# Kernel tuning notes

Measured on AMD Instinct MI355X. Metric: run time of the kernel, lower is better.

The kernel has to match this reference:

```python
import math
import jax, jax.numpy as jnp
import numpy as np

N_HEADS, INPUT_DIM, EMBED_DIM = 8, 512, 512
KEY_DIM = EMBED_DIM // N_HEADS  # 64, val_dim == key_dim
BATCH, N = 4, 2048


def setup_inputs() -> dict:
    key = jax.random.key(0)
    ks = jax.random.split(key, 6)
    def unif(k, shape):
        stdv = 1.0 / math.sqrt(shape[-1])
        return jax.random.uniform(k, shape, jnp.float32, -stdv, stdv)
    q = jax.random.normal(ks[0], (BATCH, N, INPUT_DIM), jnp.float32)
    mask = jax.random.randint(ks[1], (BATCH, N, N), 0, 2, jnp.int32)
    W_query = unif(ks[2], (N_HEADS, INPUT_DIM, KEY_DIM))
    W_key = unif(ks[3], (N_HEADS, INPUT_DIM, KEY_DIM))
    W_val = unif(ks[4], (N_HEADS, INPUT_DIM, KEY_DIM))
    W_out = unif(ks[5], (N_HEADS, KEY_DIM, EMBED_DIM))
    return {"q": q, "mask": mask, "W_query": W_query, "W_key": W_key,
            "W_val": W_val, "W_out": W_out}


def reference(q, mask, W_query, W_key, W_val, W_out):
    # Self-attention: k is None, v is None -> k = q, v = q (module forward_).
    norm = 1.0 / math.sqrt(KEY_DIM)
    m = mask.astype(bool)[None]  # (1, b, nq, ng) broadcast over heads
    Q = jnp.einsum('bnd,hdk->hbnk', q, W_query)  # (h, b, nq, dk)
    K = jnp.einsum('bnd,hdk->hbnk', q, W_key)    # (h, b, ng, dk)
    V = jnp.einsum('bnd,hdv->hbnv', q, W_val)    # (h, b, ng, dv)
    scores = norm * jnp.einsum('hbqk,hbgk->hbqg', Q, K)  # (h, b, nq, ng)
    scores = jnp.where(m, -jnp.inf, scores)
    attn = jax.nn.softmax(scores, axis=-1)
    attn = jnp.where(m, 0.0, attn)  # zero out masked (also kills NaN rows)
    heads = jnp.einsum('hbqg,hbgv->hbqv', attn, V)
    out = jnp.einsum('hbqv,hve->bqe', heads, W_out)  # (b, nq, embed)
    return out
```

## Files before the change

### kernel.cpp

```cpp
#include <hip/hip_runtime.h>
#include <hip/hip_bf16.h>
#include <stdint.h>

using bf16 = __hip_bfloat16;
typedef __attribute__((ext_vector_type(8))) short short8;
typedef __attribute__((ext_vector_type(4))) short short4b;
typedef __attribute__((ext_vector_type(4))) float f32x4;
typedef __attribute__((ext_vector_type(4))) unsigned int u32x4;

#if __has_builtin(__builtin_amdgcn_exp2f)
#define EXP2(x) __builtin_amdgcn_exp2f(x)
#else
#define EXP2(x) exp2f(x)
#endif

__device__ __forceinline__ short8 load8(const bf16* p) {
  return *reinterpret_cast<const short8*>(p);
}
__device__ __forceinline__ short f2b(float f) {
  return __builtin_bit_cast(short, __float2bfloat16(f));
}
__device__ __forceinline__ unsigned int pk2(float a, float b) {
  return (unsigned int)(unsigned short)f2b(a) |
         ((unsigned int)(unsigned short)f2b(b) << 16);
}
__device__ __forceinline__ void asy16(const bf16* g, bf16* l) {
  __builtin_amdgcn_global_load_lds(
      (const __attribute__((address_space(1))) void*)g,
      (__attribute__((address_space(3))) void*)l, 16, 0, 0);
}


__global__ void k_prep(const float4* __restrict__ x, ushort4* __restrict__ xb,
                       const float* __restrict__ Wq, const float* __restrict__ Wk,
                       const float* __restrict__ Wv, const float* __restrict__ Wo,
                       bf16* __restrict__ Wcat, bf16* __restrict__ Wot,
                       const int4* __restrict__ m4,
                       unsigned long long* __restrict__ bits) {
  int blk = blockIdx.x;
  const int tid = threadIdx.x;
  if (blk < 4096) {
    int i = blk * 256 + tid;
    float4 v = x[i];
    ushort4 o;
    o.x = (unsigned short)f2b(v.x);
    o.y = (unsigned short)f2b(v.y);
    o.z = (unsigned short)f2b(v.z);
    o.w = (unsigned short)f2b(v.w);
    xb[i] = o;
  } else if (blk < 4352) {
    int t = blk - 4096;
    __shared__ float T[64][65];
    if (t < 192) {
      int which = t >> 6;
      int h = (t >> 3) & 7, dt = t & 7;
      const float* W = (which == 0) ? Wq : ((which == 1) ? Wk : Wv);
#pragma unroll
      for (int p = 0; p < 4; ++p) {
        int row = p * 16 + (tid >> 4);
        float4 v = *(const float4*)(W + (size_t)(h * 512 + dt * 64 + row) * 64 +
                                    (tid & 15) * 4);
        T[row][(tid & 15) * 4 + 0] = v.x;
        T[row][(tid & 15) * 4 + 1] = v.y;
        T[row][(tid & 15) * 4 + 2] = v.z;
        T[row][(tid & 15) * 4 + 3] = v.w;
      }
      __syncthreads();
      float scale = (which == 0) ? 0.18033688011112042f : 1.0f;
      int jj = tid >> 2, i0 = (tid & 3) * 16;
#pragma unroll
      for (int q = 0; q < 2; ++q) {
        short8 o;
#pragma unroll
        for (int e = 0; e < 8; ++e) o[e] = f2b(T[i0 + q * 8 + e][jj] * scale);
        *(short8*)(Wcat + (size_t)(which * 512 + h * 64 + jj) * 512 + dt * 64 +
                   i0 + q * 8) = o;
      }
    } else {
      int t2 = t - 192;
      int h = t2 >> 3, et = t2 & 7;
#pragma unroll
      for (int p = 0; p < 4; ++p) {
        int row = p * 16 + (tid >> 4);
        float4 v = *(const float4*)(Wo + (size_t)(h * 64 + row) * 512 + et * 64 +
                                    (tid & 15) * 4);
        T[row][(tid & 15) * 4 + 0] = v.x;
        T[row][(tid & 15) * 4 + 1] = v.y;
        T[row][(tid & 15) * 4 + 2] = v.z;
        T[row][(tid & 15) * 4 + 3] = v.w;
      }
      __syncthreads();
      int jj = tid >> 2, i0 = (tid & 3) * 16;
#pragma unroll
      for (int q = 0; q < 2; ++q) {
        short8 o;
#pragma unroll
        for (int e = 0; e < 8; ++e) o[e] = f2b(T[i0 + q * 8 + e][jj]);
        *(short8*)(Wot + (size_t)(et * 64 + jj) * 512 + h * 64 + i0 + q * 8) = o;
      }
    }
  } else {
    int i = (blk - 4352) * 256 + tid;
    int4 v = m4[i];
    unsigned int nib = (unsigned)(v.x != 0) | ((unsigned)(v.y != 0) << 1) |
                       ((unsigned)(v.z != 0) << 2) | ((unsigned)(v.w != 0) << 3);
    unsigned long long w = (unsigned long long)nib << (4 * (tid & 15));
    w |= __shfl_xor(w, 1);
    w |= __shfl_xor(w, 2);
    w |= __shfl_xor(w, 4);
    w |= __shfl_xor(w, 8);
    if ((tid & 15) == 0) bits[i >> 4] = w;
  }
}

__device__ __forceinline__ void gemm128(const bf16* __restrict__ A,
                                        const bf16* __restrict__ Bt,
                                        bf16* As, bf16* Bs,
                                        int rowBase, int colBase,
                                        f32x4 acc[4][4]) {
  const int tid = threadIdx.x;
  const int lane = tid & 63, w = tid >> 6;
  const int g = lane >> 4, r = lane & 15;

  auto stage = [&](int buf, int s) {
#pragma unroll
    for (int p = 0; p < 2; ++p) {
      int c = p * 256 + tid;
      int row = c >> 2, gr = c & 3, sg = gr ^ (row & 3);
      asy16(A + (size_t)(rowBase + row) * 512 + s * 32 + sg * 8,
            As + buf * 4096 + c * 8);
    }
#pragma unroll
    for (int p = 0; p < 2; ++p) {
      int c = p * 256 + tid;
      int row = c >> 2, gr = c & 3, sg = gr ^ (row & 3);
      asy16(Bt + (size_t)(colBase + row) * 512 + s * 32 + sg * 8,
            Bs + buf * 4096 + c * 8);
    }
  };

  stage(0, 0);
  int buf = 0;
  const int rbl = (w >> 1) * 64, cbl = (w & 1) * 64;
  for (int s = 0; s < 16; ++s) {
    __syncthreads();
    if (s < 15) stage(buf ^ 1, s + 1);
    const bf16* a0 = As + buf * 4096;
    const bf16* b0 = Bs + buf * 4096;
    short8 af[4], bfr[4];
#pragma unroll
    for (int mt = 0; mt < 4; ++mt) {
      int row = rbl + mt * 16 + r;
      af[mt] = load8(a0 + (row * 4 + (g ^ (row & 3))) * 8);
    }
#pragma unroll
    for (int nt = 0; nt < 4; ++nt) {
      int col = cbl + nt * 16 + r;
      bfr[nt] = load8(b0 + (col * 4 + (g ^ (col & 3))) * 8);
    }
#pragma unroll
    for (int mt = 0; mt < 4; ++mt)
#pragma unroll
      for (int nt = 0; nt < 4; ++nt)
        acc[mt][nt] = __builtin_amdgcn_mfma_f32_16x16x32_bf16(
            af[mt], bfr[nt], acc[mt][nt], 0, 0, 0);
    buf ^= 1;
  }
}

__device__ __forceinline__ void gemm64x128(const bf16* __restrict__ A,
                                           const bf16* __restrict__ Bt,
                                           bf16* As, bf16* Bs,
                                           int rowBase, int colBase,
                                           f32x4 acc[2][4]) {
  const int tid = threadIdx.x;
  const int lane = tid & 63, w = tid >> 6;
  const int g = lane >> 4, r = lane & 15;

  auto stage = [&](int buf, int s) {
    {
      int c = tid;
      int row = c >> 2, gr = c & 3, sg = gr ^ (row & 3);
      asy16(A + (size_t)(rowBase + row) * 512 + s * 32 + sg * 8,
            As + buf * 2048 + c * 8);
    }
#pragma unroll
    for (int p = 0; p < 2; ++p) {
      int c = p * 256 + tid;
      int row = c >> 2, gr = c & 3, sg = gr ^ (row & 3);
      asy16(Bt + (size_t)(colBase + row) * 512 + s * 32 + sg * 8,
            Bs + buf * 4096 + c * 8);
    }
  };

  stage(0, 0);
  int buf = 0;
  const int rbl = (w >> 1) * 32, cbl = (w & 1) * 64;
  for (int s = 0; s < 16; ++s) {
    __syncthreads();
    if (s < 15) stage(buf ^ 1, s + 1);
    const bf16* a0 = As + buf * 2048;
    const bf16* b0 = Bs + buf * 4096;
    short8 af[2], bfr[4];
#pragma unroll
    for (int mt = 0; mt < 2; ++mt) {
      int row = rbl + mt * 16 + r;
      af[mt] = load8(a0 + (row * 4 + (g ^ (row & 3))) * 8);
    }
#pragma unroll
    for (int nt = 0; nt < 4; ++nt) {
      int col = cbl + nt * 16 + r;
      bfr[nt] = load8(b0 + (col * 4 + (g ^ (col & 3))) * 8);
    }
#pragma unroll
    for (int mt = 0; mt < 2; ++mt)
#pragma unroll
      for (int nt = 0; nt < 4; ++nt)
        acc[mt][nt] = __builtin_amdgcn_mfma_f32_16x16x32_bf16(
            af[mt], bfr[nt], acc[mt][nt], 0, 0, 0);
    buf ^= 1;
  }
}

__global__ __launch_bounds__(256, 3) void k_proj_qkv(
    const bf16* __restrict__ Xb, const bf16* __restrict__ Wcat,
    bf16* __restrict__ Qb, bf16* __restrict__ Kp, bf16* __restrict__ Vp) {
  __shared__ __align__(16) bf16 As[2 * 4096];
  __shared__ __align__(16) bf16 Bs[2 * 4096];
  int rowBase = blockIdx.x * 128, colBase = blockIdx.y * 128;
  f32x4 acc[4][4] = {};
  gemm128(Xb, Wcat, As, Bs, rowBase, colBase, acc);
  const int lane = threadIdx.x & 63, w = threadIdx.x >> 6;
  const int g = lane >> 4, r = lane & 15;
#pragma unroll
  for (int mt = 0; mt < 4; ++mt) {
    int row0 = rowBase + (w >> 1) * 64 + mt * 16 + 4 * g;
    int b = row0 >> 11, n0 = row0 & 2047;
    int kt = n0 >> 6;
#pragma unroll
    for (int nt = 0; nt < 4; ++nt) {
      int col = colBase + (w & 1) * 64 + nt * 16 + r;
      if (col < 512) {
        int hh = col >> 6, dk = col & 63;
        bf16* p0 = Qb + ((size_t)(b * 8 + hh) * 2048 + n0) * 64 + dk;
#pragma unroll
        for (int rr = 0; rr < 4; ++rr)
          p0[rr * 64] = __float2bfloat16(acc[mt][nt][rr]);
      } else if (col < 1024) {
        int hh = (col >> 6) & 7, dk = col & 63;
        int half = dk >> 5, gk = (dk >> 3) & 3, jj = dk & 7;
        int kr = n0 & 63;
        int kc = kr >> 4, r0 = kr & 15;
        bf16* base = Kp + (size_t)(b * 8 + hh) * 131072 + (size_t)kt * 4096 +
                     ((kc * 2 + half) * 4 + gk) * 128 + jj;
#pragma unroll
        for (int rr = 0; rr < 4; ++rr)
          base[(r0 + rr) * 8] = __float2bfloat16(acc[mt][nt][rr]);
      } else {
        int hdv = col - 1024;
        int hh = hdv >> 6, dv = hdv & 63;
        int dvs = dv >> 4, rv = dv & 15;
        int kcol0 = n0 & 63;
        int half = kcol0 >> 5, gv = (kcol0 >> 2) & 3;
        int j0 = ((kcol0 >> 4) & 1) * 4;
        short4b pkv;
#pragma unroll
        for (int rr = 0; rr < 4; ++rr) pkv[rr] = f2b(acc[mt][nt][rr]);
        *reinterpret_cast<short4b*>(
            Vp + (size_t)(b * 8 + hh) * 131072 + (size_t)kt * 4096 +
            (((half * 4 + dvs) * 4 + gv) * 16 + rv) * 8 + j0) = pkv;
      }
    }
  }
}

__global__ __launch_bounds__(256, 4) void k_proj_out(
    const bf16* __restrict__ O, const bf16* __restrict__ Wot,
    float* __restrict__ out) {
  __shared__ __align__(16) bf16 As[2 * 2048];
  __shared__ __align__(16) bf16 Bs[2 * 4096];
  int rowBase = blockIdx.x * 64, colBase = blockIdx.y * 128;
  f32x4 acc[2][4] = {};
  gemm64x128(O, Wot, As, Bs, rowBase, colBase, acc);
  const int lane = threadIdx.x & 63, w = threadIdx.x >> 6;
  const int g = lane >> 4, r = lane & 15;
#pragma unroll
  for (int mt = 0; mt < 2; ++mt) {
    int row0 = rowBase + (w >> 1) * 32 + mt * 16 + 4 * g;
#pragma unroll
    for (int nt = 0; nt < 4; ++nt) {
      int col = colBase + (w & 1) * 64 + nt * 16 + r;
#pragma unroll
      for (int rr = 0; rr < 4; ++rr)
        out[(size_t)(row0 + rr) * 512 + col] = acc[mt][nt][rr];
    }
  }
}

__global__ __launch_bounds__(512, 4) void k_attn(const bf16* __restrict__ Q,
    const bf16* __restrict__ K, const bf16* __restrict__ V,
    const unsigned long long* __restrict__ MB, bf16* __restrict__ O) {
  const int blin = blockIdx.x;
  const int j = blin >> 3;
  const int bh = (blin & 7) * 4 + (j >> 4);
  const int qt = j & 15;
  const int b = bh >> 3, h = bh & 7;
  const int tid = threadIdx.x;
  const int lane = tid & 63;
  const int wave = tid >> 6;
  const int g = lane >> 4, r = lane & 15;
  const int qbase = qt * 128 + wave * 16;

  __shared__ __align__(16) bf16 Kl[3][4096];
  __shared__ __align__(16) bf16 Vl[3][4096];

  const bf16* Kp = K + (size_t)bh * 131072;
  const bf16* Vp = V + (size_t)bh * 131072;

  short8 qf0, qf1;
  {
    const bf16* Qp = Q + ((size_t)bh * 2048 + qbase + r) * 64;
    qf0 = load8(Qp + g * 8);
    qf1 = load8(Qp + 32 + g * 8);
  }
  const unsigned long long* Mp = MB + ((size_t)b * 2048 + qbase + r) * 32;

  short8 ones;
#pragma unroll
  for (int i = 0; i < 8; ++i) ones[i] = (short)0x3F80;

  f32x4 acc[4] = {};
  f32x4 acc_l = {};

  auto stage = [&](int buf, int kt) {
    const bf16* Kg = Kp + (size_t)kt * 4096;
    const bf16* Vg = Vp + (size_t)kt * 4096;
    asy16(Kg + tid * 8, &Kl[buf][0] + tid * 8);
    asy16(Vg + tid * 8, &Vl[buf][0] + tid * 8);
  };

  auto qk = [&](const bf16* kl, f32x4 stl[4]) {
#pragma unroll
    for (int kc = 0; kc < 4; ++kc) {
      short8 kf0 = load8(kl + ((kc * 2 + 0) * 4 + g) * 128 + r * 8);
      short8 kf1 = load8(kl + ((kc * 2 + 1) * 4 + g) * 128 + r * 8);
      f32x4 z = {};
      z = __builtin_amdgcn_mfma_f32_16x16x32_bf16(kf0, qf0, z, 0, 0, 0);
      stl[kc] = __builtin_amdgcn_mfma_f32_16x16x32_bf16(kf1, qf1, z, 0, 0, 0);
    }
  };

  stage(0, 0);
  stage(1, 1);
  unsigned long long mw0, mw1;
  mw0 = Mp[0];
  __syncthreads();
  f32x4 st0[4], st1[4];
  qk(&Kl[0][0], st0);

#define ATTN_ITER(KT, CUR, NXT, STG, SC, SN, MC, MN, DO_STAGE, DO_NEXT)      \
  do {                                                                       \
    __syncthreads();                                                         \
    if (DO_STAGE) stage(STG, (KT) + 2);                                      \
    if (DO_NEXT) MN = Mp[(KT) + 1];                                          \
    __builtin_amdgcn_s_setprio(1);                                           \
    if (DO_NEXT) qk(&Kl[NXT][0], SN);                                        \
    __builtin_amdgcn_s_setprio(0);                                           \
    unsigned ml = (unsigned)MC >> (4 * g);                                   \
    unsigned mh = (unsigned)(MC >> 32) >> (4 * g);                           \
    float p[16];                                                             \
    _Pragma("unroll") for (int kc = 0; kc < 4; ++kc)                         \
        _Pragma("unroll") for (int rr = 0; rr < 4; ++rr) {                   \
      float e = EXP2(SC[kc][rr]);                                            \
      unsigned wsel = (kc & 2) ? mh : ml;                                    \
      bool bad = (wsel >> (((kc & 1) << 4) + rr)) & 1u;                      \
      p[kc * 4 + rr] = bad ? 0.f : e;                                        \
    }                                                                        \
    u32x4 q0, q1;                                                            \
    _Pragma("unroll") for (int i2 = 0; i2 < 4; ++i2) {                       \
      q0[i2] = pk2(p[2 * i2], p[2 * i2 + 1]);                                \
      q1[i2] = pk2(p[8 + 2 * i2], p[8 + 2 * i2 + 1]);                        \
    }                                                                        \
    short8 pa0 = __builtin_bit_cast(short8, q0);                             \
    short8 pa1 = __builtin_bit_cast(short8, q1);                             \
    acc_l = __builtin_amdgcn_mfma_f32_16x16x32_bf16(pa0, ones, acc_l, 0, 0, 0); \
    acc_l = __builtin_amdgcn_mfma_f32_16x16x32_bf16(pa1, ones, acc_l, 0, 0, 0); \
    const bf16* vl = &Vl[CUR][0];                                            \
    __builtin_amdgcn_s_setprio(1);                                           \
    _Pragma("unroll") for (int dvs = 0; dvs < 4; ++dvs) {                    \
      short8 vb0 = load8(vl + ((0 * 4 + dvs) * 4 + g) * 128 + r * 8);        \
      short8 vb1 = load8(vl + ((1 * 4 + dvs) * 4 + g) * 128 + r * 8);        \
      acc[dvs] = __builtin_amdgcn_mfma_f32_16x16x32_bf16(pa0, vb0, acc[dvs], 0, 0, 0); \
      acc[dvs] = __builtin_amdgcn_mfma_f32_16x16x32_bf16(pa1, vb1, acc[dvs], 0, 0, 0); \
    }                                                                        \
    __builtin_amdgcn_s_setprio(0);                                           \
  } while (0)

  for (int t = 0; t < 5; ++t) {
    const int kt = 6 * t;
    ATTN_ITER(kt + 0, 0, 1, 2, st0, st1, mw0, mw1, true, true);
    ATTN_ITER(kt + 1, 1, 2, 0, st1, st0, mw1, mw0, true, true);
    ATTN_ITER(kt + 2, 2, 0, 1, st0, st1, mw0, mw1, true, true);
    ATTN_ITER(kt + 3, 0, 1, 2, st1, st0, mw1, mw0, true, true);
    ATTN_ITER(kt + 4, 1, 2, 0, st0, st1, mw0, mw1, true, true);
    ATTN_ITER(kt + 5, 2, 0, 1, st1, st0, mw1, mw0, true, true);
  }
  ATTN_ITER(30, 0, 1, 2, st0, st1, mw0, mw1, false, true);
  ATTN_ITER(31, 1, 2, 0, st1, st0, mw1, mw0, false, false);
#undef ATTN_ITER

  float inv[4];
#pragma unroll
  for (int rr = 0; rr < 4; ++rr)
    inv[rr] = (acc_l[rr] > 0.f) ? 1.f / acc_l[rr] : 0.f;
  bf16* Op = O + ((size_t)b * 2048 + qbase + 4 * g) * 512 + h * 64;
#pragma unroll
  for (int dvs = 0; dvs < 4; ++dvs)
#pragma unroll
    for (int rr = 0; rr < 4; ++rr)
      Op[rr * 512 + dvs * 16 + r] = __float2bfloat16(acc[dvs][rr] * inv[rr]);
}


extern "C" void kernel_launch(void* const* d_in, const int* in_sizes, int n_in,
                              void* d_out, int out_size, void* d_ws, size_t ws_size,
                              hipStream_t stream) {
  const float* q    = (const float*)d_in[0];
  const int*   mask = (const int*)d_in[1];
  const float* Wq   = (const float*)d_in[2];
  const float* Wk   = (const float*)d_in[3];
  const float* Wv   = (const float*)d_in[4];
  const float* Wo   = (const float*)d_in[5];
  float* out = (float*)d_out;

  char* ws = (char*)d_ws;
  const size_t MB1 = 1024 * 1024;
  bf16* Xb   = (bf16*)(ws + 0);
  bf16* Ob   = (bf16*)(ws + 0);
  bf16* Qb   = (bf16*)(ws + 8 * MB1);
  bf16* Kpm  = (bf16*)(ws + 16 * MB1);
  bf16* Vpm  = (bf16*)(ws + 24 * MB1);
  unsigned long long* Mbits = (unsigned long long*)(ws + 32 * MB1);
  bf16* Wcat = (bf16*)(ws + 34 * MB1);
  bf16* Wot  = (bf16*)(ws + 34 * MB1 + 1536 * 512 * 2);

  k_prep<<<20736, 256, 0, stream>>>((const float4*)q, (ushort4*)Xb,
                                    Wq, Wk, Wv, Wo, Wcat, Wot,
                                    (const int4*)mask, Mbits);
  k_proj_qkv<<<dim3(64, 12), 256, 0, stream>>>(Xb, Wcat, Qb, Kpm, Vpm);
  k_attn<<<512, 512, 0, stream>>>(Qb, Kpm, Vpm, Mbits, Ob);
  k_proj_out<<<dim3(128, 4), 256, 0, stream>>>(Ob, Wot, out);
}
```

Measured before the change: 205.2 us.

## Remap GEMM blocks per XCD, invert mask bits, use packed bf16 convert

The QKV and output projection GEMMs now use a 1D grid whose block index is remapped so that each XCD handles a contiguous group of row panels, which should improve L2 reuse of the A operand. The mask bitmap is stored inverted so the attention loop can zero masked probabilities with a sign-extended bitfield AND instead of a select. Float-to-bf16 packing is done with a single v_cvt_pk_bf16_f32 instruction. The s_setprio hints around the MFMA sections are removed. Together these aim to cut VALU work in the softmax inner loop and improve cache locality, at the risk of losing the scheduling benefit that the priority hints gave.

```diff
diff --git a/kernel.cpp b/kernel.cpp
--- a/kernel.cpp
+++ b/kernel.cpp
@@ -20,9 +20,18 @@
 __device__ __forceinline__ short f2b(float f) {
   return __builtin_bit_cast(short, __float2bfloat16(f));
 }
-__device__ __forceinline__ unsigned int pk2(float a, float b) {
-  return (unsigned int)(unsigned short)f2b(a) |
-         ((unsigned int)(unsigned short)f2b(b) << 16);
+__device__ __forceinline__ unsigned int cvtpk(float lo, float hi) {
+  unsigned int r;
+  asm("v_cvt_pk_bf16_f32 %0, %1, %2" : "=v"(r) : "v"(lo), "v"(hi));
+  return r;
+}
+__device__ __forceinline__ float keepmul(float e, unsigned w, int pos) {
+#if __has_builtin(__builtin_amdgcn_sbfe)
+  unsigned km = (unsigned)__builtin_amdgcn_sbfe((int)w, pos, 1);
+  return __builtin_bit_cast(float, __builtin_bit_cast(unsigned, e) & km);
+#else
+  return ((w >> pos) & 1u) ? e : 0.f;
+#endif
 }
 __device__ __forceinline__ void asy16(const bf16* g, bf16* l) {
   __builtin_amdgcn_global_load_lds(
@@ -109,7 +118,7 @@
     w |= __shfl_xor(w, 2);
     w |= __shfl_xor(w, 4);
     w |= __shfl_xor(w, 8);
-    if ((tid & 15) == 0) bits[i >> 4] = w;
+    if ((tid & 15) == 0) bits[i >> 4] = ~w;
   }
 }
 
@@ -225,9 +234,13 @@
 __global__ __launch_bounds__(256, 3) void k_proj_qkv(
     const bf16* __restrict__ Xb, const bf16* __restrict__ Wcat,
     bf16* __restrict__ Qb, bf16* __restrict__ Kp, bf16* __restrict__ Vp) {
+  const int bid = blockIdx.x;
+  const int xcd = bid & 7, idx = bid >> 3;
+  const int rowPanel = (xcd << 3) | (idx & 7);
+  const int colPanel = idx >> 3;
+  int rowBase = rowPanel * 128, colBase = colPanel * 128;
   __shared__ __align__(16) bf16 As[2 * 4096];
   __shared__ __align__(16) bf16 Bs[2 * 4096];
-  int rowBase = blockIdx.x * 128, colBase = blockIdx.y * 128;
   f32x4 acc[4][4] = {};
   gemm128(Xb, Wcat, As, Bs, rowBase, colBase, acc);
   const int lane = threadIdx.x & 63, w = threadIdx.x >> 6;
@@ -277,9 +290,13 @@
 __global__ __launch_bounds__(256, 4) void k_proj_out(
     const bf16* __restrict__ O, const bf16* __restrict__ Wot,
     float* __restrict__ out) {
+  const int bid = blockIdx.x;
+  const int xcd = bid & 7, idx = bid >> 3;
+  const int rowPanel = (xcd << 4) | (idx & 15);
+  const int colPanel = idx >> 4;
+  int rowBase = rowPanel * 64, colBase = colPanel * 128;
   __shared__ __align__(16) bf16 As[2 * 2048];
   __shared__ __align__(16) bf16 Bs[2 * 4096];
-  int rowBase = blockIdx.x * 64, colBase = blockIdx.y * 128;
   f32x4 acc[2][4] = {};
   gemm64x128(O, Wot, As, Bs, rowBase, colBase, acc);
   const int lane = threadIdx.x & 63, w = threadIdx.x >> 6;
@@ -358,42 +375,35 @@
   f32x4 st0[4], st1[4];
   qk(&Kl[0][0], st0);
 
-#define ATTN_ITER(KT, CUR, NXT, STG, SC, SN, MC, MN, DO_STAGE, DO_NEXT)      \
-  do {                                                                       \
-    __syncthreads();                                                         \
-    if (DO_STAGE) stage(STG, (KT) + 2);                                      \
-    if (DO_NEXT) MN = Mp[(KT) + 1];                                          \
-    __builtin_amdgcn_s_setprio(1);                                           \
-    if (DO_NEXT) qk(&Kl[NXT][0], SN);                                        \
-    __builtin_amdgcn_s_setprio(0);                                           \
-    unsigned ml = (unsigned)MC >> (4 * g);                                   \
-    unsigned mh = (unsigned)(MC >> 32) >> (4 * g);                           \
-    float p[16];                                                             \
-    _Pragma("unroll") for (int kc = 0; kc < 4; ++kc)                         \
-        _Pragma("unroll") for (int rr = 0; rr < 4; ++rr) {                   \
-      float e = EXP2(SC[kc][rr]);                                            \
-      unsigned wsel = (kc & 2) ? mh : ml;                                    \
-      bool bad = (wsel >> (((kc & 1) << 4) + rr)) & 1u;                      \
-      p[kc * 4 + rr] = bad ? 0.f : e;                                        \
-    }                                                                        \
-    u32x4 q0, q1;                                                            \
-    _Pragma("unroll") for (int i2 = 0; i2 < 4; ++i2) {                       \
-      q0[i2] = pk2(p[2 * i2], p[2 * i2 + 1]);                                \
-      q1[i2] = pk2(p[8 + 2 * i2], p[8 + 2 * i2 + 1]);                        \
-    }                                                                        \
-    short8 pa0 = __builtin_bit_cast(short8, q0);                             \
-    short8 pa1 = __builtin_bit_cast(short8, q1);                             \
+#define ATTN_ITER(KT, CUR, NXT, STG, SC, SN, MC, MN, DO_STAGE, DO_NEXT)       \
+  do {                                                                        \
+    __syncthreads();                                                          \
+    if (DO_STAGE) stage(STG, (KT) + 2);                                       \
+    if (DO_NEXT) MN = Mp[(KT) + 1];                                           \
+    if (DO_NEXT) qk(&Kl[NXT][0], SN);                                         \
+    unsigned ml = (unsigned)MC >> (4 * g);                                    \
+    unsigned mh = (unsigned)(MC >> 32) >> (4 * g);                            \
+    float p[16];                                                              \
+    _Pragma("unroll") for (int kc = 0; kc < 4; ++kc)                          \
+        _Pragma("unroll") for (int rr = 0; rr < 4; ++rr)                      \
+      p[kc * 4 + rr] = keepmul(EXP2(SC[kc][rr]), (kc & 2) ? mh : ml,          \
+                               ((kc & 1) << 4) + rr);                         \
+    u32x4 q0, q1;                                                             \
+    _Pragma("unroll") for (int i2 = 0; i2 < 4; ++i2) {                        \
+      q0[i2] = cvtpk(p[2 * i2], p[2 * i2 + 1]);                               \
+      q1[i2] = cvtpk(p[8 + 2 * i2], p[8 + 2 * i2 + 1]);                       \
+    }                                                                         \
+    short8 pa0 = __builtin_bit_cast(short8, q0);                              \
+    short8 pa1 = __builtin_bit_cast(short8, q1);                              \
     acc_l = __builtin_amdgcn_mfma_f32_16x16x32_bf16(pa0, ones, acc_l, 0, 0, 0); \
     acc_l = __builtin_amdgcn_mfma_f32_16x16x32_bf16(pa1, ones, acc_l, 0, 0, 0); \
-    const bf16* vl = &Vl[CUR][0];                                            \
-    __builtin_amdgcn_s_setprio(1);                                           \
-    _Pragma("unroll") for (int dvs = 0; dvs < 4; ++dvs) {                    \
-      short8 vb0 = load8(vl + ((0 * 4 + dvs) * 4 + g) * 128 + r * 8);        \
-      short8 vb1 = load8(vl + ((1 * 4 + dvs) * 4 + g) * 128 + r * 8);        \
+    const bf16* vl = &Vl[CUR][0];                                             \
+    _Pragma("unroll") for (int dvs = 0; dvs < 4; ++dvs) {                     \
+      short8 vb0 = load8(vl + ((0 * 4 + dvs) * 4 + g) * 128 + r * 8);         \
+      short8 vb1 = load8(vl + ((1 * 4 + dvs) * 4 + g) * 128 + r * 8);         \
       acc[dvs] = __builtin_amdgcn_mfma_f32_16x16x32_bf16(pa0, vb0, acc[dvs], 0, 0, 0); \
       acc[dvs] = __builtin_amdgcn_mfma_f32_16x16x32_bf16(pa1, vb1, acc[dvs], 0, 0, 0); \
-    }                                                                        \
-    __builtin_amdgcn_s_setprio(0);                                           \
+    }                                                                         \
   } while (0)
 
   for (int t = 0; t < 5; ++t) {
@@ -447,7 +457,7 @@
   k_prep<<<20736, 256, 0, stream>>>((const float4*)q, (ushort4*)Xb,
                                     Wq, Wk, Wv, Wo, Wcat, Wot,
                                     (const int4*)mask, Mbits);
-  k_proj_qkv<<<dim3(64, 12), 256, 0, stream>>>(Xb, Wcat, Qb, Kpm, Vpm);
+  k_proj_qkv<<<768, 256, 0, stream>>>(Xb, Wcat, Qb, Kpm, Vpm);
   k_attn<<<512, 512, 0, stream>>>(Qb, Kpm, Vpm, Mbits, Ob);
-  k_proj_out<<<dim3(128, 4), 256, 0, stream>>>(Ob, Wot, out);
-}
+  k_proj_out<<<512, 256, 0, stream>>>(Ob, Wot, out);
+}
```

Measured after the change: 200.4 us. 1.02x faster.
